# Performance work log

Hardware: AMD Instinct MI355X
Metric: run time of the kernel (lower is better)

Reference implementation:

```python
import jax, jax.numpy as jnp
import numpy as np

N_HEADS, N_KV, HEAD_DIM, D_MODEL, T_MAX = 16, 4, 64, 1024, 2048
GROUPS = N_HEADS // N_KV
EPS = 1e-6


def _rms_norm(x, w):
    # RMSNorm over last dim (head_dim), computed in fp32 like the torch module
    xf = x.astype(jnp.float32)
    r = jax.lax.rsqrt(jnp.mean(xf * xf, axis=-1, keepdims=True) + EPS)
    return (xf * r).astype(x.dtype) * w


def _apply_rope(x, cos, sin):
    # x: (B, H, T, D); cos/sin: (T_max, D/2)
    T = x.shape[2]
    c = cos[:T][None, None]  # (1,1,T,D/2)
    s = sin[:T][None, None]
    x1, x2 = jnp.split(x, 2, axis=-1)
    return jnp.concatenate([x1 * c - x2 * s, x2 * c + x1 * s], axis=-1)


def setup_inputs() -> dict:
    key = jax.random.key(0)
    ks = jax.random.split(key, 8)
    B, T = 2, 2048
    x = jax.random.normal(ks[0], (B, T, D_MODEL), dtype=jnp.float32)
    # realistic RoPE tables
    theta = 10000.0
    inv_freq = 1.0 / (theta ** (np.arange(0, HEAD_DIM, 2, dtype=np.float32) / HEAD_DIM))
    t = np.arange(T_MAX, dtype=np.float32)
    freqs = np.outer(t, inv_freq)  # (T_max, D/2)
    cos = jnp.asarray(np.cos(freqs))
    sin = jnp.asarray(np.sin(freqs))
    sd = 0.02
    wq = jax.random.normal(ks[1], (N_HEADS * HEAD_DIM, D_MODEL), dtype=jnp.float32) * sd
    wk = jax.random.normal(ks[2], (N_KV * HEAD_DIM, D_MODEL), dtype=jnp.float32) * sd
    wv = jax.random.normal(ks[3], (N_KV * HEAD_DIM, D_MODEL), dtype=jnp.float32) * sd
    wo = jax.random.normal(ks[4], (D_MODEL, N_HEADS * HEAD_DIM), dtype=jnp.float32) * sd
    qn_w = jnp.ones((HEAD_DIM,), dtype=jnp.float32)
    kn_w = jnp.ones((HEAD_DIM,), dtype=jnp.float32)
    return {"x": x, "cos": cos, "sin": sin, "wq": wq, "wk": wk, "wv": wv,
            "wo": wo, "qn_w": qn_w, "kn_w": kn_w}


def reference(x, cos, sin, wq, wk, wv, wo, qn_w, kn_w):
    B, T, _ = x.shape
    scale = HEAD_DIM ** -0.5
    # projections (torch Linear: y = x @ W.T)
    q = (x @ wq.T).reshape(B, T, N_HEADS, HEAD_DIM).transpose(0, 2, 1, 3)
    k = (x @ wk.T).reshape(B, T, N_KV, HEAD_DIM).transpose(0, 2, 1, 3)
    v = (x @ wv.T).reshape(B, T, N_KV, HEAD_DIM).transpose(0, 2, 1, 3)
    # qk RMSNorm
    q = _rms_norm(q, qn_w)
    k = _rms_norm(k, kn_w)
    # RoPE
    q = _apply_rope(q, cos, sin)
    k = _apply_rope(k, cos, sin)
    # GQA expansion: query head h uses kv head h // GROUPS
    k = jnp.repeat(k, GROUPS, axis=1)  # (B, H, T, D)
    v = jnp.repeat(v, GROUPS, axis=1)
    # causal SDPA
    scores = jnp.einsum('bhqd,bhkd->bhqk', q, k) * scale
    causal = jnp.tril(jnp.ones((T, T), dtype=bool))
    scores = jnp.where(causal, scores, jnp.finfo(scores.dtype).min)
    p = jax.nn.softmax(scores, axis=-1)
    out = jnp.einsum('bhqk,bhkd->bhqd', p, v)
    out = out.transpose(0, 2, 1, 3).reshape(B, T, N_HEADS * HEAD_DIM)
    return out @ wo.T
```

## Files before the change

### kernel.cpp

```cpp
#include <hip/hip_runtime.h>


typedef __bf16 bf16;
typedef __attribute__((ext_vector_type(8))) __bf16 bf16x8;
typedef __attribute__((ext_vector_type(4))) float f32x4;

#define MFMA(a, b, c) __builtin_amdgcn_mfma_f32_16x16x32_bf16((a), (b), (c), 0, 0, 0)
#define GLOAD_LDS16(g, l)                                        \
  __builtin_amdgcn_global_load_lds(                              \
      (const __attribute__((address_space(1))) void*)(g),        \
      (__attribute__((address_space(3))) void*)(l), 16, 0, 0)

__device__ __forceinline__ bool is_bf16_input(const void* cosRaw) {
  return ((const unsigned short*)cosRaw)[0] == 0x3F80;
}
__device__ __forceinline__ float rdval(const void* p, int idx, bool isbf) {
  return isbf ? (float)((const bf16*)p)[idx] : ((const float*)p)[idx];
}

__device__ __forceinline__ void stage_rows(const void* src, size_t rowbase,
                                           int K, int ko, int srow, int csrc,
                                           int lane, bf16* ls, bool isbf) {
  if (isbf) {
    GLOAD_LDS16(&((const bf16*)src)[(rowbase + srow) * K + ko + csrc * 8], ls);
  } else {
    const float* fp = &((const float*)src)[(rowbase + srow) * K + ko + csrc * 8];
    float4 f0 = *(const float4*)fp;
    float4 f1 = *(const float4*)(fp + 4);
    bf16x8 o;
    o[0] = (bf16)f0.x; o[1] = (bf16)f0.y; o[2] = (bf16)f0.z; o[3] = (bf16)f0.w;
    o[4] = (bf16)f1.x; o[5] = (bf16)f1.y; o[6] = (bf16)f1.z; o[7] = (bf16)f1.w;
    *(bf16x8*)&ls[lane * 8] = o;
  }
}

__global__ __launch_bounds__(256, 3) void proj_kernel(
    const void* __restrict__ xraw, const void* __restrict__ wqraw,
    const void* __restrict__ wkraw, const void* __restrict__ wvraw,
    bf16* __restrict__ qp, bf16* __restrict__ kp, bf16* __restrict__ vt,
    const void* __restrict__ cosraw, const void* __restrict__ sinraw,
    const void* __restrict__ qnraw, const void* __restrict__ knraw) {
  __shared__ bf16 As[2][128 * 64];
  __shared__ bf16 Bs[2][64 * 64];

  const int idx = (int)blockIdx.x;
  const int xcd = idx & 7;
  const int jj = idx >> 3;
  const int mb = (jj & 3) * 8 + xcd;
  const int nb = jj >> 2;
  const int n0 = nb * 64;
  const int m0 = mb * 128;

  const int tid = threadIdx.x;
  const int wave = tid >> 6;
  const int lane = tid & 63;
  const int q16 = lane & 15;
  const int quad = lane >> 4;
  const int srow = lane >> 3;
  const int csrc = (lane & 7) ^ srow;
  const int wm = wave * 32;
  const int x7 = q16 & 7;
  const bool isbf = is_bf16_input(cosraw);

  const void* wsrc;
  int nr0;
  if (nb < 16)      { wsrc = wqraw; nr0 = n0; }
  else if (nb < 20) { wsrc = wkraw; nr0 = n0 - 1024; }
  else              { wsrc = wvraw; nr0 = n0 - 1280; }

  auto stage = [&](int ko, int bb) {
#pragma unroll
    for (int i = 0; i < 4; ++i) {
      int rb = wave * 32 + i * 8;
      stage_rows(xraw, (size_t)(m0 + rb), 1024, ko, srow, csrc, lane,
                 &As[bb][rb * 64], isbf);
    }
#pragma unroll
    for (int i = 0; i < 2; ++i) {
      int rb = wave * 16 + i * 8;
      stage_rows(wsrc, (size_t)(nr0 + rb), 1024, ko, srow, csrc, lane,
                 &Bs[bb][rb * 64], isbf);
    }
  };

  f32x4 acc[2][4];
#pragma unroll
  for (int mt = 0; mt < 2; ++mt)
#pragma unroll
    for (int nt = 0; nt < 4; ++nt) acc[mt][nt] = (f32x4){0.f, 0.f, 0.f, 0.f};

  stage(0, 0);

  for (int kt = 0; kt < 16; ++kt) {
    const int bb = kt & 1;
    __syncthreads();
    if (kt + 1 < 16) stage((kt + 1) * 64, bb ^ 1);

    bf16x8 af[2][2], bfr[4][2];
#pragma unroll
    for (int mt = 0; mt < 2; ++mt) {
      const bf16* rp = &As[bb][(wm + mt * 16 + q16) * 64];
      af[mt][0] = *(const bf16x8*)&rp[(quad ^ x7) * 8];
      af[mt][1] = *(const bf16x8*)&rp[((quad + 4) ^ x7) * 8];
    }
#pragma unroll
    for (int nt = 0; nt < 4; ++nt) {
      const bf16* rp = &Bs[bb][(nt * 16 + q16) * 64];
      bfr[nt][0] = *(const bf16x8*)&rp[(quad ^ x7) * 8];
      bfr[nt][1] = *(const bf16x8*)&rp[((quad + 4) ^ x7) * 8];
    }
#pragma unroll
    for (int mt = 0; mt < 2; ++mt)
#pragma unroll
      for (int nt = 0; nt < 4; ++nt) {
        acc[mt][nt] = MFMA(af[mt][0], bfr[nt][0], acc[mt][nt]);
        acc[mt][nt] = MFMA(af[mt][1], bfr[nt][1], acc[mt][nt]);
      }
  }
  __syncthreads();

  if (nb < 20) {
    const void* nwp = (nb < 16) ? qnraw : knraw;
    const float osc = (nb < 16) ? 0.125f : 1.0f;
    float wd[4];
#pragma unroll
    for (int nt = 0; nt < 4; ++nt) wd[nt] = rdval(nwp, nt * 16 + q16, isbf);

#pragma unroll
    for (int mt = 0; mt < 2; ++mt)
#pragma unroll
      for (int r = 0; r < 4; ++r) {
        float p = acc[mt][0][r] * acc[mt][0][r] + acc[mt][1][r] * acc[mt][1][r] +
                  acc[mt][2][r] * acc[mt][2][r] + acc[mt][3][r] * acc[mt][3][r];
#pragma unroll
        for (int off = 8; off >= 1; off >>= 1) p += __shfl_xor(p, off);
        float rms = rsqrtf(p * (1.0f / 64.0f) + 1e-6f);

        int row = m0 + wm + mt * 16 + quad * 4 + r;
        int t = row & 2047;
        float c0 = rdval(cosraw, t * 32 + q16, isbf);
        float c1 = rdval(cosraw, t * 32 + 16 + q16, isbf);
        float s0 = rdval(sinraw, t * 32 + q16, isbf);
        float s1 = rdval(sinraw, t * 32 + 16 + q16, isbf);

        float v0 = acc[mt][0][r] * rms * wd[0];
        float v1 = acc[mt][1][r] * rms * wd[1];
        float v2 = acc[mt][2][r] * rms * wd[2];
        float v3 = acc[mt][3][r] * rms * wd[3];

        bf16* op = (nb < 16) ? &qp[(size_t)row * 1024 + nb * 64]
                             : &kp[(size_t)row * 256 + (nb - 16) * 64];
        op[0 * 16 + q16] = (bf16)((v0 * c0 - v2 * s0) * osc);
        op[1 * 16 + q16] = (bf16)((v1 * c1 - v3 * s1) * osc);
        op[2 * 16 + q16] = (bf16)((v2 * c0 + v0 * s0) * osc);
        op[3 * 16 + q16] = (bf16)((v3 * c1 + v1 * s1) * osc);
      }
  } else {
    const int vh = nb - 20;
    const int b = m0 >> 11;
    const int tbase = (m0 & 2047) + wm;
    bf16* tb = &As[0][wave * 2048];
#pragma unroll
    for (int mt = 0; mt < 2; ++mt)
#pragma unroll
      for (int nt = 0; nt < 4; ++nt)
#pragma unroll
        for (int r = 0; r < 4; ++r)
          tb[(mt * 16 + quad * 4 + r) * 64 + nt * 16 + q16] = (bf16)acc[mt][nt][r];
#pragma unroll
    for (int rep = 0; rep < 4; ++rep) {
      int c = lane + 64 * rep;
      int d = c >> 2;
      int t8 = (c & 3) * 8;
      bf16x8 pk;
#pragma unroll
      for (int j = 0; j < 8; ++j) pk[j] = tb[(t8 + j) * 64 + d];
      *(bf16x8*)&vt[(((size_t)(b * 4 + vh)) * 64 + d) * 2048 + tbase + t8] = pk;
    }
  }
}

__global__ __launch_bounds__(256, 2) void flash_kernel(
    const bf16* __restrict__ qp, const bf16* __restrict__ kp,
    const bf16* __restrict__ vt, bf16* __restrict__ attn) {
  const int qblk = blockIdx.z ? 31 - (int)blockIdx.x : (int)blockIdx.x;
  const int hp = blockIdx.y;
  const int b = blockIdx.z;
  const int h0 = hp * 2;
  const int kvh = hp >> 1;
  const int tid = threadIdx.x;
  const int wave = tid >> 6;
  const int lane = tid & 63;
  const int q16 = lane & 15;
  const int quad = lane >> 4;
  const int r7 = q16 & 7;
  const int t0 = qblk * 64 + wave * 16;

  __shared__ bf16 Ks[2][64 * 64];
  __shared__ bf16 Vs[2][64 * 64];
  __shared__ bf16 Pl[4][2][16 * 64];

  bf16x8 qa[2][2];
#pragma unroll
  for (int hd = 0; hd < 2; ++hd) {
    const bf16* qrow =
        qp + (((size_t)(b * 2048 + t0 + q16)) * 16 + h0 + hd) * 64;
    qa[hd][0] = *(const bf16x8*)(qrow + quad * 8);
    qa[hd][1] = *(const bf16x8*)(qrow + 32 + quad * 8);
  }

  bf16x8 ones;
#pragma unroll
  for (int j = 0; j < 8; ++j) ones[j] = (bf16)1.0f;

  f32x4 O[2][4], l4[2];
#pragma unroll
  for (int hd = 0; hd < 2; ++hd) {
#pragma unroll
    for (int nt = 0; nt < 4; ++nt) O[hd][nt] = (f32x4){0.f, 0.f, 0.f, 0.f};
    l4[hd] = (f32x4){0.f, 0.f, 0.f, 0.f};
  }

  const int ntile = qblk + 1;

  bf16x8 kr[2], vr[2];
  const int cr = tid * 2;
  const int krow = cr >> 3;
  const size_t kgbase = (((size_t)(b * 2048) + krow) * 4 + kvh) * 64;
  const size_t vgbase = ((size_t)(b * 4 + kvh) * 64 + krow) * 2048;

  auto gload = [&](int tk) {
#pragma unroll
    for (int rep = 0; rep < 2; ++rep) {
      int ch = (cr + rep) & 7;
      kr[rep] = *(const bf16x8*)&kp[kgbase + (size_t)(tk * 64) * 256 + ch * 8];
      vr[rep] = *(const bf16x8*)&vt[vgbase + tk * 64 + ch * 8];
    }
  };
  auto swrite = [&](int bb) {
#pragma unroll
    for (int rep = 0; rep < 2; ++rep) {
      int ch = (cr + rep) & 7;
      int pos = (ch ^ (krow & 7)) * 8;
      *(bf16x8*)&Ks[bb][krow * 64 + pos] = kr[rep];
      *(bf16x8*)&Vs[bb][krow * 64 + pos] = vr[rep];
    }
  };

  gload(0);

  for (int t = 0; t < ntile; ++t) {
    const int bb = t & 1;
    const int kbase = t * 64;
    swrite(bb);
    __syncthreads();
    if (t + 1 < ntile) gload(t + 1);

    bf16x8 vbr[2][4];
#pragma unroll
    for (int kh = 0; kh < 2; ++kh)
#pragma unroll
      for (int nt = 0; nt < 4; ++nt) {
        const bf16* vr0 = &Vs[bb][(nt * 16 + q16) * 64];
        vbr[kh][nt] = *(const bf16x8*)&vr0[((kh * 4 + quad) ^ r7) * 8];
      }

    bf16x8 kb[4][2];
#pragma unroll
    for (int kt = 0; kt < 4; ++kt) {
      const bf16* kr0 = &Ks[bb][(kt * 16 + q16) * 64];
      kb[kt][0] = *(const bf16x8*)&kr0[(quad ^ r7) * 8];
      kb[kt][1] = *(const bf16x8*)&kr0[((quad + 4) ^ r7) * 8];
    }

    const bool edge = (kbase + 63 > t0);
#pragma unroll
    for (int hd = 0; hd < 2; ++hd) {
      f32x4 s[4];
#pragma unroll
      for (int kt = 0; kt < 4; ++kt) {
        f32x4 z = (f32x4){0.f, 0.f, 0.f, 0.f};
        z = MFMA(qa[hd][0], kb[kt][0], z);
        z = MFMA(qa[hd][1], kb[kt][1], z);
        s[kt] = z;
      }
      if (edge) {
#pragma unroll
        for (int kt = 0; kt < 4; ++kt) {
          int jt = kbase + kt * 16 + q16;
#pragma unroll
          for (int r = 0; r < 4; ++r)
            if (jt > t0 + quad * 4 + r) s[kt][r] = -1e30f;
        }
      }
#pragma unroll
      for (int kt = 0; kt < 4; ++kt)
#pragma unroll
        for (int r = 0; r < 4; ++r) s[kt][r] = __expf(s[kt][r] - 9.0f);

#pragma unroll
      for (int kt = 0; kt < 4; ++kt)
#pragma unroll
        for (int r = 0; r < 4; ++r) {
          int row = quad * 4 + r;
          int col = kt * 16 + q16;
          Pl[wave][hd][row * 64 + ((col >> 3) ^ (row & 7)) * 8 + (col & 7)] =
              (bf16)s[kt][r];
        }
    }

#pragma unroll
    for (int hd = 0; hd < 2; ++hd)
#pragma unroll
      for (int kh = 0; kh < 2; ++kh) {
        bf16x8 pa = *(const bf16x8*)&Pl[wave][hd][q16 * 64 +
                                                  (((kh * 4 + quad) ^ r7) * 8)];
#pragma unroll
        for (int nt = 0; nt < 4; ++nt)
          O[hd][nt] = MFMA(pa, vbr[kh][nt], O[hd][nt]);
        l4[hd] = MFMA(pa, ones, l4[hd]);
      }
  }

#pragma unroll
  for (int hd = 0; hd < 2; ++hd) {
    float inv[4];
#pragma unroll
    for (int r = 0; r < 4; ++r) inv[r] = 1.0f / l4[hd][r];
#pragma unroll
    for (int nt = 0; nt < 4; ++nt)
#pragma unroll
      for (int r = 0; r < 4; ++r) {
        size_t o = (((size_t)(b * 2048 + t0 + quad * 4 + r)) * 16 + h0 + hd) * 64 +
                   nt * 16 + q16;
        attn[o] = (bf16)(O[hd][nt][r] * inv[r]);
      }
  }
}

__global__ __launch_bounds__(256, 2) void gemm_o_kernel(
    const bf16* __restrict__ A, const void* __restrict__ Wraw,
    void* __restrict__ C, const void* __restrict__ cosraw) {
  __shared__ bf16 As[2][128 * 64];
  __shared__ bf16 Bs[2][64 * 64];

  const int idx = (int)blockIdx.x;
  const int xcd = idx & 7;
  const int jj = idx >> 3;
  const int mb = (jj & 3) * 8 + xcd;
  const int nb = jj >> 2;
  const int n0 = nb * 64;
  const int m0 = mb * 128;

  const int tid = threadIdx.x;
  const int wave = tid >> 6;
  const int lane = tid & 63;
  const int q16 = lane & 15;
  const int quad = lane >> 4;
  const int srow = lane >> 3;
  const int csrc = (lane & 7) ^ srow;
  const int wm = wave * 32;
  const int x7 = q16 & 7;
  const bool isbf = is_bf16_input(cosraw);

  auto stage = [&](int ko, int bb) {
#pragma unroll
    for (int i = 0; i < 4; ++i) {
      int rb = wave * 32 + i * 8;
      GLOAD_LDS16(&A[(size_t)(m0 + rb + srow) * 1024 + ko + csrc * 8],
                  &As[bb][rb * 64]);
    }
#pragma unroll
    for (int i = 0; i < 2; ++i) {
      int rb = wave * 16 + i * 8;
      stage_rows(Wraw, (size_t)(n0 + rb), 1024, ko, srow, csrc, lane,
                 &Bs[bb][rb * 64], isbf);
    }
  };

  f32x4 acc[2][4];
#pragma unroll
  for (int mt = 0; mt < 2; ++mt)
#pragma unroll
    for (int nt = 0; nt < 4; ++nt) acc[mt][nt] = (f32x4){0.f, 0.f, 0.f, 0.f};

  stage(0, 0);

  for (int kt = 0; kt < 16; ++kt) {
    const int bb = kt & 1;
    __syncthreads();
    if (kt + 1 < 16) stage((kt + 1) * 64, bb ^ 1);

    bf16x8 af[2][2], bfr[4][2];
#pragma unroll
    for (int mt = 0; mt < 2; ++mt) {
      const bf16* rp = &As[bb][(wm + mt * 16 + q16) * 64];
      af[mt][0] = *(const bf16x8*)&rp[(quad ^ x7) * 8];
      af[mt][1] = *(const bf16x8*)&rp[((quad + 4) ^ x7) * 8];
    }
#pragma unroll
    for (int nt = 0; nt < 4; ++nt) {
      const bf16* rp = &Bs[bb][(nt * 16 + q16) * 64];
      bfr[nt][0] = *(const bf16x8*)&rp[(quad ^ x7) * 8];
      bfr[nt][1] = *(const bf16x8*)&rp[((quad + 4) ^ x7) * 8];
    }
#pragma unroll
    for (int mt = 0; mt < 2; ++mt)
#pragma unroll
      for (int nt = 0; nt < 4; ++nt) {
        acc[mt][nt] = MFMA(af[mt][0], bfr[nt][0], acc[mt][nt]);
        acc[mt][nt] = MFMA(af[mt][1], bfr[nt][1], acc[mt][nt]);
      }
  }

#pragma unroll
  for (int mt = 0; mt < 2; ++mt)
#pragma unroll
    for (int nt = 0; nt < 4; ++nt)
#pragma unroll
      for (int r = 0; r < 4; ++r) {
        size_t idx2 = (size_t)(m0 + wm + mt * 16 + quad * 4 + r) * 1024 +
                      n0 + nt * 16 + q16;
        if (isbf) ((bf16*)C)[idx2] = (bf16)acc[mt][nt][r];
        else      ((float*)C)[idx2] = acc[mt][nt][r];
      }
}

extern "C" void kernel_launch(void* const* d_in, const int* in_sizes, int n_in,
                              void* d_out, int out_size, void* d_ws, size_t ws_size,
                              hipStream_t stream) {
  bf16* qp = (bf16*)d_ws;
  bf16* kp = qp + (size_t)4096 * 1024;
  bf16* vt = kp + (size_t)4096 * 256;
  bf16* at = vt + (size_t)4096 * 256;

  proj_kernel<<<768, 256, 0, stream>>>(
      d_in[0], d_in[3], d_in[4], d_in[5], qp, kp, vt,
      d_in[1], d_in[2], d_in[7], d_in[8]);

  flash_kernel<<<dim3(32, 8, 2), 256, 0, stream>>>(qp, kp, vt, at);

  gemm_o_kernel<<<512, 256, 0, stream>>>(at, d_in[6], d_out, d_in[1]);
}
```

Baseline: 189.7 us.

## Load GEMM fragments directly from global memory into registers, bypassing LDS

The projection and output GEMM kernels no longer stage A and W tiles through double-buffered shared memory. Each lane now loads its MFMA fragments straight from global memory, with register double buffering, which removes the LDS round trip and the per-iteration block barriers. The cost is that fragments shared across waves are loaded redundantly: the weight tile is fetched by all four waves. The per-lane accesses are also strided by whole rows instead of coalesced, so more L2 traffic and less efficient memory transactions are likely.

```diff
diff --git a/kernel.cpp b/kernel.cpp
--- a/kernel.cpp
+++ b/kernel.cpp
@@ -6,10 +6,6 @@
 typedef __attribute__((ext_vector_type(4))) float f32x4;
 
 #define MFMA(a, b, c) __builtin_amdgcn_mfma_f32_16x16x32_bf16((a), (b), (c), 0, 0, 0)
-#define GLOAD_LDS16(g, l)                                        \
-  __builtin_amdgcn_global_load_lds(                              \
-      (const __attribute__((address_space(1))) void*)(g),        \
-      (__attribute__((address_space(3))) void*)(l), 16, 0, 0)
 
 __device__ __forceinline__ bool is_bf16_input(const void* cosRaw) {
   return ((const unsigned short*)cosRaw)[0] == 0x3F80;
@@ -18,20 +14,15 @@
   return isbf ? (float)((const bf16*)p)[idx] : ((const float*)p)[idx];
 }
 
-__device__ __forceinline__ void stage_rows(const void* src, size_t rowbase,
-                                           int K, int ko, int srow, int csrc,
-                                           int lane, bf16* ls, bool isbf) {
-  if (isbf) {
-    GLOAD_LDS16(&((const bf16*)src)[(rowbase + srow) * K + ko + csrc * 8], ls);
-  } else {
-    const float* fp = &((const float*)src)[(rowbase + srow) * K + ko + csrc * 8];
-    float4 f0 = *(const float4*)fp;
-    float4 f1 = *(const float4*)(fp + 4);
-    bf16x8 o;
-    o[0] = (bf16)f0.x; o[1] = (bf16)f0.y; o[2] = (bf16)f0.z; o[3] = (bf16)f0.w;
-    o[4] = (bf16)f1.x; o[5] = (bf16)f1.y; o[6] = (bf16)f1.z; o[7] = (bf16)f1.w;
-    *(bf16x8*)&ls[lane * 8] = o;
-  }
+__device__ __forceinline__ bf16x8 ldfrag(const void* p, size_t ei, bool isbf) {
+  if (isbf) return *(const bf16x8*)((const bf16*)p + ei);
+  const float* fp = (const float*)p + ei;
+  float4 f0 = *(const float4*)fp;
+  float4 f1 = *(const float4*)(fp + 4);
+  bf16x8 o;
+  o[0] = (bf16)f0.x; o[1] = (bf16)f0.y; o[2] = (bf16)f0.z; o[3] = (bf16)f0.w;
+  o[4] = (bf16)f1.x; o[5] = (bf16)f1.y; o[6] = (bf16)f1.z; o[7] = (bf16)f1.w;
+  return o;
 }
 
 __global__ __launch_bounds__(256, 3) void proj_kernel(
@@ -40,8 +31,7 @@
     bf16* __restrict__ qp, bf16* __restrict__ kp, bf16* __restrict__ vt,
     const void* __restrict__ cosraw, const void* __restrict__ sinraw,
     const void* __restrict__ qnraw, const void* __restrict__ knraw) {
-  __shared__ bf16 As[2][128 * 64];
-  __shared__ bf16 Bs[2][64 * 64];
+  __shared__ bf16 tbuf[4 * 2048];
 
   const int idx = (int)blockIdx.x;
   const int xcd = idx & 7;
@@ -56,10 +46,7 @@
   const int lane = tid & 63;
   const int q16 = lane & 15;
   const int quad = lane >> 4;
-  const int srow = lane >> 3;
-  const int csrc = (lane & 7) ^ srow;
   const int wm = wave * 32;
-  const int x7 = q16 & 7;
   const bool isbf = is_bf16_input(cosraw);
 
   const void* wsrc;
@@ -68,20 +55,13 @@
   else if (nb < 20) { wsrc = wkraw; nr0 = n0 - 1024; }
   else              { wsrc = wvraw; nr0 = n0 - 1280; }
 
-  auto stage = [&](int ko, int bb) {
-#pragma unroll
-    for (int i = 0; i < 4; ++i) {
-      int rb = wave * 32 + i * 8;
-      stage_rows(xraw, (size_t)(m0 + rb), 1024, ko, srow, csrc, lane,
-                 &As[bb][rb * 64], isbf);
-    }
-#pragma unroll
-    for (int i = 0; i < 2; ++i) {
-      int rb = wave * 16 + i * 8;
-      stage_rows(wsrc, (size_t)(nr0 + rb), 1024, ko, srow, csrc, lane,
-                 &Bs[bb][rb * 64], isbf);
-    }
-  };
+  size_t abase[2], wbase[4];
+#pragma unroll
+  for (int mt = 0; mt < 2; ++mt)
+    abase[mt] = (size_t)(m0 + wm + mt * 16 + q16) * 1024 + quad * 8;
+#pragma unroll
+  for (int nt = 0; nt < 4; ++nt)
+    wbase[nt] = (size_t)(nr0 + nt * 16 + q16) * 1024 + quad * 8;
 
   f32x4 acc[2][4];
 #pragma unroll
@@ -89,35 +69,45 @@
 #pragma unroll
     for (int nt = 0; nt < 4; ++nt) acc[mt][nt] = (f32x4){0.f, 0.f, 0.f, 0.f};
 
-  stage(0, 0);
-
+  bf16x8 ac[2][2], bc[4][2], an[2][2], bn[4][2];
+#pragma unroll
+  for (int mt = 0; mt < 2; ++mt) {
+    ac[mt][0] = ldfrag(xraw, abase[mt], isbf);
+    ac[mt][1] = ldfrag(xraw, abase[mt] + 32, isbf);
+  }
+#pragma unroll
+  for (int nt = 0; nt < 4; ++nt) {
+    bc[nt][0] = ldfrag(wsrc, wbase[nt], isbf);
+    bc[nt][1] = ldfrag(wsrc, wbase[nt] + 32, isbf);
+  }
+
+#pragma unroll
   for (int kt = 0; kt < 16; ++kt) {
-    const int bb = kt & 1;
-    __syncthreads();
-    if (kt + 1 < 16) stage((kt + 1) * 64, bb ^ 1);
-
-    bf16x8 af[2][2], bfr[4][2];
-#pragma unroll
-    for (int mt = 0; mt < 2; ++mt) {
-      const bf16* rp = &As[bb][(wm + mt * 16 + q16) * 64];
-      af[mt][0] = *(const bf16x8*)&rp[(quad ^ x7) * 8];
-      af[mt][1] = *(const bf16x8*)&rp[((quad + 4) ^ x7) * 8];
-    }
-#pragma unroll
-    for (int nt = 0; nt < 4; ++nt) {
-      const bf16* rp = &Bs[bb][(nt * 16 + q16) * 64];
-      bfr[nt][0] = *(const bf16x8*)&rp[(quad ^ x7) * 8];
-      bfr[nt][1] = *(const bf16x8*)&rp[((quad + 4) ^ x7) * 8];
+    if (kt + 1 < 16) {
+      const int kn = (kt + 1) * 64;
+#pragma unroll
+      for (int mt = 0; mt < 2; ++mt) {
+        an[mt][0] = ldfrag(xraw, abase[mt] + kn, isbf);
+        an[mt][1] = ldfrag(xraw, abase[mt] + kn + 32, isbf);
+      }
+#pragma unroll
+      for (int nt = 0; nt < 4; ++nt) {
+        bn[nt][0] = ldfrag(wsrc, wbase[nt] + kn, isbf);
+        bn[nt][1] = ldfrag(wsrc, wbase[nt] + kn + 32, isbf);
+      }
     }
 #pragma unroll
     for (int mt = 0; mt < 2; ++mt)
 #pragma unroll
       for (int nt = 0; nt < 4; ++nt) {
-        acc[mt][nt] = MFMA(af[mt][0], bfr[nt][0], acc[mt][nt]);
-        acc[mt][nt] = MFMA(af[mt][1], bfr[nt][1], acc[mt][nt]);
-      }
-  }
-  __syncthreads();
+        acc[mt][nt] = MFMA(ac[mt][0], bc[nt][0], acc[mt][nt]);
+        acc[mt][nt] = MFMA(ac[mt][1], bc[nt][1], acc[mt][nt]);
+      }
+#pragma unroll
+    for (int mt = 0; mt < 2; ++mt) { ac[mt][0] = an[mt][0]; ac[mt][1] = an[mt][1]; }
+#pragma unroll
+    for (int nt = 0; nt < 4; ++nt) { bc[nt][0] = bn[nt][0]; bc[nt][1] = bn[nt][1]; }
+  }
 
   if (nb < 20) {
     const void* nwp = (nb < 16) ? qnraw : knraw;
@@ -159,7 +149,7 @@
     const int vh = nb - 20;
     const int b = m0 >> 11;
     const int tbase = (m0 & 2047) + wm;
-    bf16* tb = &As[0][wave * 2048];
+    bf16* tb = &tbuf[wave * 2048];
 #pragma unroll
     for (int mt = 0; mt < 2; ++mt)
 #pragma unroll
@@ -341,9 +331,6 @@
 __global__ __launch_bounds__(256, 2) void gemm_o_kernel(
     const bf16* __restrict__ A, const void* __restrict__ Wraw,
     void* __restrict__ C, const void* __restrict__ cosraw) {
-  __shared__ bf16 As[2][128 * 64];
-  __shared__ bf16 Bs[2][64 * 64];
-
   const int idx = (int)blockIdx.x;
   const int xcd = idx & 7;
   const int jj = idx >> 3;
@@ -357,26 +344,16 @@
   const int lane = tid & 63;
   const int q16 = lane & 15;
   const int quad = lane >> 4;
-  const int srow = lane >> 3;
-  const int csrc = (lane & 7) ^ srow;
   const int wm = wave * 32;
-  const int x7 = q16 & 7;
   const bool isbf = is_bf16_input(cosraw);
 
-  auto stage = [&](int ko, int bb) {
-#pragma unroll
-    for (int i = 0; i < 4; ++i) {
-      int rb = wave * 32 + i * 8;
-      GLOAD_LDS16(&A[(size_t)(m0 + rb + srow) * 1024 + ko + csrc * 8],
-                  &As[bb][rb * 64]);
-    }
-#pragma unroll
-    for (int i = 0; i < 2; ++i) {
-      int rb = wave * 16 + i * 8;
-      stage_rows(Wraw, (size_t)(n0 + rb), 1024, ko, srow, csrc, lane,
-                 &Bs[bb][rb * 64], isbf);
-    }
-  };
+  size_t abase[2], wbase[4];
+#pragma unroll
+  for (int mt = 0; mt < 2; ++mt)
+    abase[mt] = (size_t)(m0 + wm + mt * 16 + q16) * 1024 + quad * 8;
+#pragma unroll
+  for (int nt = 0; nt < 4; ++nt)
+    wbase[nt] = (size_t)(n0 + nt * 16 + q16) * 1024 + quad * 8;
 
   f32x4 acc[2][4];
 #pragma unroll
@@ -384,33 +361,44 @@
 #pragma unroll
     for (int nt = 0; nt < 4; ++nt) acc[mt][nt] = (f32x4){0.f, 0.f, 0.f, 0.f};
 
-  stage(0, 0);
-
+  bf16x8 ac[2][2], bc[4][2], an[2][2], bn[4][2];
+#pragma unroll
+  for (int mt = 0; mt < 2; ++mt) {
+    ac[mt][0] = *(const bf16x8*)&A[abase[mt]];
+    ac[mt][1] = *(const bf16x8*)&A[abase[mt] + 32];
+  }
+#pragma unroll
+  for (int nt = 0; nt < 4; ++nt) {
+    bc[nt][0] = ldfrag(Wraw, wbase[nt], isbf);
+    bc[nt][1] = ldfrag(Wraw, wbase[nt] + 32, isbf);
+  }
+
+#pragma unroll
   for (int kt = 0; kt < 16; ++kt) {
-    const int bb = kt & 1;
-    __syncthreads();
-    if (kt + 1 < 16) stage((kt + 1) * 64, bb ^ 1);
-
-    bf16x8 af[2][2], bfr[4][2];
-#pragma unroll
-    for (int mt = 0; mt < 2; ++mt) {
-      const bf16* rp = &As[bb][(wm + mt * 16 + q16) * 64];
-      af[mt][0] = *(const bf16x8*)&rp[(quad ^ x7) * 8];
-      af[mt][1] = *(const bf16x8*)&rp[((quad + 4) ^ x7) * 8];
-    }
-#pragma unroll
-    for (int nt = 0; nt < 4; ++nt) {
-      const bf16* rp = &Bs[bb][(nt * 16 + q16) * 64];
-      bfr[nt][0] = *(const bf16x8*)&rp[(quad ^ x7) * 8];
-      bfr[nt][1] = *(const bf16x8*)&rp[((quad + 4) ^ x7) * 8];
+    if (kt + 1 < 16) {
+      const int kn = (kt + 1) * 64;
+#pragma unroll
+      for (int mt = 0; mt < 2; ++mt) {
+        an[mt][0] = *(const bf16x8*)&A[abase[mt] + kn];
+        an[mt][1] = *(const bf16x8*)&A[abase[mt] + kn + 32];
+      }
+#pragma unroll
+      for (int nt = 0; nt < 4; ++nt) {
+        bn[nt][0] = ldfrag(Wraw, wbase[nt] + kn, isbf);
+        bn[nt][1] = ldfrag(Wraw, wbase[nt] + kn + 32, isbf);
+      }
     }
 #pragma unroll
     for (int mt = 0; mt < 2; ++mt)
 #pragma unroll
       for (int nt = 0; nt < 4; ++nt) {
-        acc[mt][nt] = MFMA(af[mt][0], bfr[nt][0], acc[mt][nt]);
-        acc[mt][nt] = MFMA(af[mt][1], bfr[nt][1], acc[mt][nt]);
-      }
+        acc[mt][nt] = MFMA(ac[mt][0], bc[nt][0], acc[mt][nt]);
+        acc[mt][nt] = MFMA(ac[mt][1], bc[nt][1], acc[mt][nt]);
+      }
+#pragma unroll
+    for (int mt = 0; mt < 2; ++mt) { ac[mt][0] = an[mt][0]; ac[mt][1] = an[mt][1]; }
+#pragma unroll
+    for (int nt = 0; nt < 4; ++nt) { bc[nt][0] = bn[nt][0]; bc[nt][1] = bn[nt][1]; }
   }
 
 #pragma unroll
```

After: 323.3 us. 1.7x slower.

## Shrink projection and output GEMM tiles to 64x64, single-buffered, for occupancy

Applied to the files above, without the earlier changes.

Both the QKV projection and output projection GEMMs move from 128x64 double-buffered tiles to 64x64 single-buffered tiles. This doubles the grid size and raises launch-bound occupancy from 2-3 to 6 blocks per CU. The goal is more parallelism and better latency hiding through occupancy rather than software prefetch. In exchange, staging loads are no longer overlapped with MFMA inside a block, each tile reuses its loaded data less, and there is an extra barrier per k-step.

```diff
diff --git a/kernel.cpp b/kernel.cpp
--- a/kernel.cpp
+++ b/kernel.cpp
@@ -19,12 +19,12 @@
 }
 
 __device__ __forceinline__ void stage_rows(const void* src, size_t rowbase,
-                                           int K, int ko, int srow, int csrc,
+                                           int ko, int srow, int csrc,
                                            int lane, bf16* ls, bool isbf) {
   if (isbf) {
-    GLOAD_LDS16(&((const bf16*)src)[(rowbase + srow) * K + ko + csrc * 8], ls);
+    GLOAD_LDS16(&((const bf16*)src)[(rowbase + srow) * 1024 + ko + csrc * 8], ls);
   } else {
-    const float* fp = &((const float*)src)[(rowbase + srow) * K + ko + csrc * 8];
+    const float* fp = &((const float*)src)[(rowbase + srow) * 1024 + ko + csrc * 8];
     float4 f0 = *(const float4*)fp;
     float4 f1 = *(const float4*)(fp + 4);
     bf16x8 o;
@@ -34,22 +34,22 @@
   }
 }
 
-__global__ __launch_bounds__(256, 3) void proj_kernel(
+__global__ __launch_bounds__(256, 6) void proj_kernel(
     const void* __restrict__ xraw, const void* __restrict__ wqraw,
     const void* __restrict__ wkraw, const void* __restrict__ wvraw,
     bf16* __restrict__ qp, bf16* __restrict__ kp, bf16* __restrict__ vt,
     const void* __restrict__ cosraw, const void* __restrict__ sinraw,
     const void* __restrict__ qnraw, const void* __restrict__ knraw) {
-  __shared__ bf16 As[2][128 * 64];
-  __shared__ bf16 Bs[2][64 * 64];
+  __shared__ bf16 As[64 * 64];
+  __shared__ bf16 Bs[64 * 64];
 
   const int idx = (int)blockIdx.x;
   const int xcd = idx & 7;
   const int jj = idx >> 3;
-  const int mb = (jj & 3) * 8 + xcd;
-  const int nb = jj >> 2;
+  const int mb = (jj & 7) * 8 + xcd;
+  const int nb = jj >> 3;
   const int n0 = nb * 64;
-  const int m0 = mb * 128;
+  const int m0 = mb * 64;
 
   const int tid = threadIdx.x;
   const int wave = tid >> 6;
@@ -58,7 +58,7 @@
   const int quad = lane >> 4;
   const int srow = lane >> 3;
   const int csrc = (lane & 7) ^ srow;
-  const int wm = wave * 32;
+  const int wm = wave * 16;
   const int x7 = q16 & 7;
   const bool isbf = is_bf16_input(cosraw);
 
@@ -68,56 +68,39 @@
   else if (nb < 20) { wsrc = wkraw; nr0 = n0 - 1024; }
   else              { wsrc = wvraw; nr0 = n0 - 1280; }
 
-  auto stage = [&](int ko, int bb) {
-#pragma unroll
-    for (int i = 0; i < 4; ++i) {
-      int rb = wave * 32 + i * 8;
-      stage_rows(xraw, (size_t)(m0 + rb), 1024, ko, srow, csrc, lane,
-                 &As[bb][rb * 64], isbf);
-    }
+  f32x4 acc[4];
+#pragma unroll
+  for (int nt = 0; nt < 4; ++nt) acc[nt] = (f32x4){0.f, 0.f, 0.f, 0.f};
+
+  for (int kt = 0; kt < 16; ++kt) {
+    const int ko = kt * 64;
 #pragma unroll
     for (int i = 0; i < 2; ++i) {
       int rb = wave * 16 + i * 8;
-      stage_rows(wsrc, (size_t)(nr0 + rb), 1024, ko, srow, csrc, lane,
-                 &Bs[bb][rb * 64], isbf);
-    }
-  };
-
-  f32x4 acc[2][4];
-#pragma unroll
-  for (int mt = 0; mt < 2; ++mt)
-#pragma unroll
-    for (int nt = 0; nt < 4; ++nt) acc[mt][nt] = (f32x4){0.f, 0.f, 0.f, 0.f};
-
-  stage(0, 0);
-
-  for (int kt = 0; kt < 16; ++kt) {
-    const int bb = kt & 1;
-    __syncthreads();
-    if (kt + 1 < 16) stage((kt + 1) * 64, bb ^ 1);
-
-    bf16x8 af[2][2], bfr[4][2];
-#pragma unroll
-    for (int mt = 0; mt < 2; ++mt) {
-      const bf16* rp = &As[bb][(wm + mt * 16 + q16) * 64];
-      af[mt][0] = *(const bf16x8*)&rp[(quad ^ x7) * 8];
-      af[mt][1] = *(const bf16x8*)&rp[((quad + 4) ^ x7) * 8];
+      stage_rows(xraw, (size_t)(m0 + rb), ko, srow, csrc, lane, &As[rb * 64], isbf);
+      stage_rows(wsrc, (size_t)(nr0 + rb), ko, srow, csrc, lane, &Bs[rb * 64], isbf);
+    }
+    __syncthreads();
+
+    bf16x8 a0, a1, bfr[4][2];
+    {
+      const bf16* rp = &As[(wm + q16) * 64];
+      a0 = *(const bf16x8*)&rp[(quad ^ x7) * 8];
+      a1 = *(const bf16x8*)&rp[((quad + 4) ^ x7) * 8];
     }
 #pragma unroll
     for (int nt = 0; nt < 4; ++nt) {
-      const bf16* rp = &Bs[bb][(nt * 16 + q16) * 64];
+      const bf16* rp = &Bs[(nt * 16 + q16) * 64];
       bfr[nt][0] = *(const bf16x8*)&rp[(quad ^ x7) * 8];
       bfr[nt][1] = *(const bf16x8*)&rp[((quad + 4) ^ x7) * 8];
     }
 #pragma unroll
-    for (int mt = 0; mt < 2; ++mt)
-#pragma unroll
-      for (int nt = 0; nt < 4; ++nt) {
-        acc[mt][nt] = MFMA(af[mt][0], bfr[nt][0], acc[mt][nt]);
-        acc[mt][nt] = MFMA(af[mt][1], bfr[nt][1], acc[mt][nt]);
-      }
-  }
-  __syncthreads();
+    for (int nt = 0; nt < 4; ++nt) {
+      acc[nt] = MFMA(a0, bfr[nt][0], acc[nt]);
+      acc[nt] = MFMA(a1, bfr[nt][1], acc[nt]);
+    }
+    __syncthreads();
+  }
 
   if (nb < 20) {
     const void* nwp = (nb < 16) ? qnraw : knraw;
@@ -127,54 +110,50 @@
     for (int nt = 0; nt < 4; ++nt) wd[nt] = rdval(nwp, nt * 16 + q16, isbf);
 
 #pragma unroll
-    for (int mt = 0; mt < 2; ++mt)
-#pragma unroll
-      for (int r = 0; r < 4; ++r) {
-        float p = acc[mt][0][r] * acc[mt][0][r] + acc[mt][1][r] * acc[mt][1][r] +
-                  acc[mt][2][r] * acc[mt][2][r] + acc[mt][3][r] * acc[mt][3][r];
-#pragma unroll
-        for (int off = 8; off >= 1; off >>= 1) p += __shfl_xor(p, off);
-        float rms = rsqrtf(p * (1.0f / 64.0f) + 1e-6f);
-
-        int row = m0 + wm + mt * 16 + quad * 4 + r;
-        int t = row & 2047;
-        float c0 = rdval(cosraw, t * 32 + q16, isbf);
-        float c1 = rdval(cosraw, t * 32 + 16 + q16, isbf);
-        float s0 = rdval(sinraw, t * 32 + q16, isbf);
-        float s1 = rdval(sinraw, t * 32 + 16 + q16, isbf);
-
-        float v0 = acc[mt][0][r] * rms * wd[0];
-        float v1 = acc[mt][1][r] * rms * wd[1];
-        float v2 = acc[mt][2][r] * rms * wd[2];
-        float v3 = acc[mt][3][r] * rms * wd[3];
-
-        bf16* op = (nb < 16) ? &qp[(size_t)row * 1024 + nb * 64]
-                             : &kp[(size_t)row * 256 + (nb - 16) * 64];
-        op[0 * 16 + q16] = (bf16)((v0 * c0 - v2 * s0) * osc);
-        op[1 * 16 + q16] = (bf16)((v1 * c1 - v3 * s1) * osc);
-        op[2 * 16 + q16] = (bf16)((v2 * c0 + v0 * s0) * osc);
-        op[3 * 16 + q16] = (bf16)((v3 * c1 + v1 * s1) * osc);
-      }
+    for (int r = 0; r < 4; ++r) {
+      float p = acc[0][r] * acc[0][r] + acc[1][r] * acc[1][r] +
+                acc[2][r] * acc[2][r] + acc[3][r] * acc[3][r];
+#pragma unroll
+      for (int off = 8; off >= 1; off >>= 1) p += __shfl_xor(p, off);
+      float rms = rsqrtf(p * (1.0f / 64.0f) + 1e-6f);
+
+      int row = m0 + wm + quad * 4 + r;
+      int t = row & 2047;
+      float c0 = rdval(cosraw, t * 32 + q16, isbf);
+      float c1 = rdval(cosraw, t * 32 + 16 + q16, isbf);
+      float s0 = rdval(sinraw, t * 32 + q16, isbf);
+      float s1 = rdval(sinraw, t * 32 + 16 + q16, isbf);
+
+      float v0 = acc[0][r] * rms * wd[0];
+      float v1 = acc[1][r] * rms * wd[1];
+      float v2 = acc[2][r] * rms * wd[2];
+      float v3 = acc[3][r] * rms * wd[3];
+
+      bf16* op = (nb < 16) ? &qp[(size_t)row * 1024 + nb * 64]
+                           : &kp[(size_t)row * 256 + (nb - 16) * 64];
+      op[0 * 16 + q16] = (bf16)((v0 * c0 - v2 * s0) * osc);
+      op[1 * 16 + q16] = (bf16)((v1 * c1 - v3 * s1) * osc);
+      op[2 * 16 + q16] = (bf16)((v2 * c0 + v0 * s0) * osc);
+      op[3 * 16 + q16] = (bf16)((v3 * c1 + v1 * s1) * osc);
+    }
   } else {
     const int vh = nb - 20;
     const int b = m0 >> 11;
-    const int tbase = (m0 & 2047) + wm;
-    bf16* tb = &As[0][wave * 2048];
-#pragma unroll
-    for (int mt = 0; mt < 2; ++mt)
-#pragma unroll
-      for (int nt = 0; nt < 4; ++nt)
-#pragma unroll
-        for (int r = 0; r < 4; ++r)
-          tb[(mt * 16 + quad * 4 + r) * 64 + nt * 16 + q16] = (bf16)acc[mt][nt][r];
-#pragma unroll
-    for (int rep = 0; rep < 4; ++rep) {
-      int c = lane + 64 * rep;
-      int d = c >> 2;
-      int t8 = (c & 3) * 8;
+    const int tbase = m0 & 2047;
+#pragma unroll
+    for (int nt = 0; nt < 4; ++nt)
+#pragma unroll
+      for (int r = 0; r < 4; ++r)
+        As[(wm + quad * 4 + r) * 64 + nt * 16 + q16] = (bf16)acc[nt][r];
+    __syncthreads();
+#pragma unroll
+    for (int rep = 0; rep < 2; ++rep) {
+      int c = tid + 256 * rep;
+      int d = c >> 3;
+      int t8 = (c & 7) * 8;
       bf16x8 pk;
 #pragma unroll
-      for (int j = 0; j < 8; ++j) pk[j] = tb[(t8 + j) * 64 + d];
+      for (int j = 0; j < 8; ++j) pk[j] = As[(t8 + j) * 64 + d];
       *(bf16x8*)&vt[(((size_t)(b * 4 + vh)) * 64 + d) * 2048 + tbase + t8] = pk;
     }
   }
@@ -338,19 +317,19 @@
   }
 }
 
-__global__ __launch_bounds__(256, 2) void gemm_o_kernel(
+__global__ __launch_bounds__(256, 6) void gemm_o_kernel(
     const bf16* __restrict__ A, const void* __restrict__ Wraw,
     void* __restrict__ C, const void* __restrict__ cosraw) {
-  __shared__ bf16 As[2][128 * 64];
-  __shared__ bf16 Bs[2][64 * 64];
+  __shared__ bf16 As[64 * 64];
+  __shared__ bf16 Bs[64 * 64];
 
   const int idx = (int)blockIdx.x;
   const int xcd = idx & 7;
   const int jj = idx >> 3;
-  const int mb = (jj & 3) * 8 + xcd;
-  const int nb = jj >> 2;
+  const int mb = (jj & 7) * 8 + xcd;
+  const int nb = jj >> 3;
   const int n0 = nb * 64;
-  const int m0 = mb * 128;
+  const int m0 = mb * 64;
 
   const int tid = threadIdx.x;
   const int wave = tid >> 6;
@@ -359,71 +338,53 @@
   const int quad = lane >> 4;
   const int srow = lane >> 3;
   const int csrc = (lane & 7) ^ srow;
-  const int wm = wave * 32;
+  const int wm = wave * 16;
   const int x7 = q16 & 7;
   const bool isbf = is_bf16_input(cosraw);
 
-  auto stage = [&](int ko, int bb) {
-#pragma unroll
-    for (int i = 0; i < 4; ++i) {
-      int rb = wave * 32 + i * 8;
-      GLOAD_LDS16(&A[(size_t)(m0 + rb + srow) * 1024 + ko + csrc * 8],
-                  &As[bb][rb * 64]);
-    }
+  f32x4 acc[4];
+#pragma unroll
+  for (int nt = 0; nt < 4; ++nt) acc[nt] = (f32x4){0.f, 0.f, 0.f, 0.f};
+
+  for (int kt = 0; kt < 16; ++kt) {
+    const int ko = kt * 64;
 #pragma unroll
     for (int i = 0; i < 2; ++i) {
       int rb = wave * 16 + i * 8;
-      stage_rows(Wraw, (size_t)(n0 + rb), 1024, ko, srow, csrc, lane,
-                 &Bs[bb][rb * 64], isbf);
-    }
-  };
-
-  f32x4 acc[2][4];
-#pragma unroll
-  for (int mt = 0; mt < 2; ++mt)
-#pragma unroll
-    for (int nt = 0; nt < 4; ++nt) acc[mt][nt] = (f32x4){0.f, 0.f, 0.f, 0.f};
-
-  stage(0, 0);
-
-  for (int kt = 0; kt < 16; ++kt) {
-    const int bb = kt & 1;
-    __syncthreads();
-    if (kt + 1 < 16) stage((kt + 1) * 64, bb ^ 1);
-
-    bf16x8 af[2][2], bfr[4][2];
-#pragma unroll
-    for (int mt = 0; mt < 2; ++mt) {
-      const bf16* rp = &As[bb][(wm + mt * 16 + q16) * 64];
-      af[mt][0] = *(const bf16x8*)&rp[(quad ^ x7) * 8];
-      af[mt][1] = *(const bf16x8*)&rp[((quad + 4) ^ x7) * 8];
+      GLOAD_LDS16(&A[(size_t)(m0 + rb + srow) * 1024 + ko + csrc * 8],
+                  &As[rb * 64]);
+      stage_rows(Wraw, (size_t)(n0 + rb), ko, srow, csrc, lane, &Bs[rb * 64], isbf);
+    }
+    __syncthreads();
+
+    bf16x8 a0, a1, bfr[4][2];
+    {
+      const bf16* rp = &As[(wm + q16) * 64];
+      a0 = *(const bf16x8*)&rp[(quad ^ x7) * 8];
+      a1 = *(const bf16x8*)&rp[((quad + 4) ^ x7) * 8];
     }
 #pragma unroll
     for (int nt = 0; nt < 4; ++nt) {
-      const bf16* rp = &Bs[bb][(nt * 16 + q16) * 64];
+      const bf16* rp = &Bs[(nt * 16 + q16) * 64];
       bfr[nt][0] = *(const bf16x8*)&rp[(quad ^ x7) * 8];
       bfr[nt][1] = *(const bf16x8*)&rp[((quad + 4) ^ x7) * 8];
     }
 #pragma unroll
-    for (int mt = 0; mt < 2; ++mt)
-#pragma unroll
-      for (int nt = 0; nt < 4; ++nt) {
-        acc[mt][nt] = MFMA(af[mt][0], bfr[nt][0], acc[mt][nt]);
-        acc[mt][nt] = MFMA(af[mt][1], bfr[nt][1], acc[mt][nt]);
-      }
-  }
-
-#pragma unroll
-  for (int mt = 0; mt < 2; ++mt)
-#pragma unroll
-    for (int nt = 0; nt < 4; ++nt)
-#pragma unroll
-      for (int r = 0; r < 4; ++r) {
-        size_t idx2 = (size_t)(m0 + wm + mt * 16 + quad * 4 + r) * 1024 +
-                      n0 + nt * 16 + q16;
-        if (isbf) ((bf16*)C)[idx2] = (bf16)acc[mt][nt][r];
-        else      ((float*)C)[idx2] = acc[mt][nt][r];
-      }
+    for (int nt = 0; nt < 4; ++nt) {
+      acc[nt] = MFMA(a0, bfr[nt][0], acc[nt]);
+      acc[nt] = MFMA(a1, bfr[nt][1], acc[nt]);
+    }
+    __syncthreads();
+  }
+
+#pragma unroll
+  for (int nt = 0; nt < 4; ++nt)
+#pragma unroll
+    for (int r = 0; r < 4; ++r) {
+      size_t idx2 = (size_t)(m0 + wm + quad * 4 + r) * 1024 + n0 + nt * 16 + q16;
+      if (isbf) ((bf16*)C)[idx2] = (bf16)acc[nt][r];
+      else      ((float*)C)[idx2] = acc[nt][r];
+    }
 }
 
 extern "C" void kernel_launch(void* const* d_in, const int* in_sizes, int n_in,
@@ -434,11 +395,11 @@
   bf16* vt = kp + (size_t)4096 * 256;
   bf16* at = vt + (size_t)4096 * 256;
 
-  proj_kernel<<<768, 256, 0, stream>>>(
+  proj_kernel<<<1536, 256, 0, stream>>>(
       d_in[0], d_in[3], d_in[4], d_in[5], qp, kp, vt,
       d_in[1], d_in[2], d_in[7], d_in[8]);
 
   flash_kernel<<<dim3(32, 8, 2), 256, 0, stream>>>(qp, kp, vt, at);
 
-  gemm_o_kernel<<<512, 256, 0, stream>>>(at, d_in[6], d_out, d_in[1]);
-}
+  gemm_o_kernel<<<1024, 256, 0, stream>>>(at, d_in[6], d_out, d_in[1]);
+}
```

Result: faster. 176.8 us (-6.8%).
